# Optimization experiments

Measured on AMD Instinct MI355X. Metric: run time of the kernel, lower is better.

Reference implementation:

```python
import jax, jax.numpy as jnp
import numpy as np

B, N, K = 4, 65536, 16
HIDDEN = 64


def setup_inputs() -> dict:
    key = jax.random.key(0)
    k1, k2, k3, k4 = jax.random.split(key, 4)
    pos = jax.random.normal(k1, (B, 3, N), dtype=jnp.float32)
    idx = jax.random.randint(k2, (B, N, K), 0, N, dtype=jnp.int64)
    dist = jax.random.uniform(k3, (B, N, K), dtype=jnp.float32)
    W = jax.random.normal(k4, (10, HIDDEN), dtype=jnp.float32) * (1.0 / np.sqrt(10.0))
    b = jnp.zeros((HIDDEN,), dtype=jnp.float32)
    return {"pos": pos, "idx": idx, "dist": dist, "W": W, "b": b}


def reference(pos, idx, dist, W, b):
    xyz = pos[:, :3, :]                                  # [B, 3, N]
    # gather neighbor coords: neighbors[b, c, n, k] = xyz[b, c, idx[b, n, k]]
    neighbors = jax.vmap(lambda x, i: x[:, i])(xyz, idx)  # [B, 3, N, K]
    ext_xyz = jnp.broadcast_to(xyz[:, :, :, None], neighbors.shape)
    concat = jnp.concatenate(
        [ext_xyz, neighbors, ext_xyz - neighbors, dist[:, None, :, :]], axis=1
    )                                                    # [B, 10, N, K]
    feat = jnp.max(concat, axis=-1)                      # [B, 10, N]
    feat = jnp.transpose(feat, (0, 2, 1))                # [B, N, 10]
    return jax.nn.relu(feat @ W + b)                     # [B, N, HIDDEN]
```

## Files before the change

### kernel.cpp

```cpp
#include <hip/hip_runtime.h>

#define NPTS 65536
#define NB_SHIFT 16
#define HID 64

typedef float vfloat4 __attribute__((ext_vector_type(4)));
typedef int   vint4   __attribute__((ext_vector_type(4)));

__global__ __launch_bounds__(256) void xyzt_kernel(const float* __restrict__ pos,
                                                   vfloat4* __restrict__ xyzt) {
    int g = blockIdx.x * 256 + threadIdx.x;
    int b = g >> NB_SHIFT;
    int n = g & (NPTS - 1);
    const float* p = pos + (size_t)b * 3 * NPTS;
    vfloat4 v;
    v.x = p[n];
    v.y = p[n + NPTS];
    v.z = p[n + 2 * NPTS];
    v.w = 0.f;
    xyzt[((size_t)b << NB_SHIFT) + n] = v;
}

template <int USE_T>
__global__ __launch_bounds__(256, 4) void point_embed_kernel(
    const float*   __restrict__ pos,
    const vfloat4* __restrict__ xyzt,
    const int*     __restrict__ idx,
    const float*   __restrict__ dist,
    const float*   __restrict__ W,
    const float*   __restrict__ bias,
    float*         __restrict__ out) {
    __shared__ float featS[10][256];
    const int tid = threadIdx.x;

    const int blk = ((int)blockIdx.x & 7) * 128 + ((int)blockIdx.x >> 3);
    const int g = blk * 256 + tid;
    const int b = g >> NB_SHIFT;
    const int n = g & (NPTS - 1);

    const vint4* iv = (const vint4*)idx + (size_t)g * 4;
    vint4 i0 = iv[0], i1 = iv[1], i2 = iv[2], i3 = iv[3];

    float cx, cy, cz;
    float mxx = -INFINITY, mxy = -INFINITY, mxz = -INFINITY;
    float mnx = INFINITY, mny = INFINITY, mnz = INFINITY;
    float maxd;

    if (USE_T) {
        const vfloat4* xb = xyzt + ((size_t)b << NB_SHIFT);
        vfloat4 c = xb[n];
        vfloat4 q[16];
        q[0]  = xb[(unsigned)i0.x];
        q[1]  = xb[(unsigned)i0.y];
        q[2]  = xb[(unsigned)i0.z];
        q[3]  = xb[(unsigned)i0.w];
        q[4]  = xb[(unsigned)i1.x];
        q[5]  = xb[(unsigned)i1.y];
        q[6]  = xb[(unsigned)i1.z];
        q[7]  = xb[(unsigned)i1.w];
        q[8]  = xb[(unsigned)i2.x];
        q[9]  = xb[(unsigned)i2.y];
        q[10] = xb[(unsigned)i2.z];
        q[11] = xb[(unsigned)i2.w];
        q[12] = xb[(unsigned)i3.x];
        q[13] = xb[(unsigned)i3.y];
        q[14] = xb[(unsigned)i3.z];
        q[15] = xb[(unsigned)i3.w];

        const vfloat4* dv = (const vfloat4*)dist + (size_t)g * 4;
        vfloat4 d0 = dv[0], d1 = dv[1], d2 = dv[2], d3 = dv[3];
        maxd = fmaxf(
            fmaxf(fmaxf(fmaxf(d0.x, d0.y), fmaxf(d0.z, d0.w)),
                  fmaxf(fmaxf(d1.x, d1.y), fmaxf(d1.z, d1.w))),
            fmaxf(fmaxf(fmaxf(d2.x, d2.y), fmaxf(d2.z, d2.w)),
                  fmaxf(fmaxf(d3.x, d3.y), fmaxf(d3.z, d3.w))));

        cx = c.x; cy = c.y; cz = c.z;
#pragma unroll
        for (int j = 0; j < 16; ++j) {
            mxx = fmaxf(mxx, q[j].x);
            mxy = fmaxf(mxy, q[j].y);
            mxz = fmaxf(mxz, q[j].z);
            mnx = fminf(mnx, q[j].x);
            mny = fminf(mny, q[j].y);
            mnz = fminf(mnz, q[j].z);
        }
    } else {
        const float* px = pos + (size_t)b * 3 * NPTS;
        cx = px[n]; cy = px[n + NPTS]; cz = px[n + 2 * NPTS];
        const vfloat4* dv = (const vfloat4*)dist + (size_t)g * 4;
        vfloat4 d0 = dv[0], d1 = dv[1], d2 = dv[2], d3 = dv[3];
        maxd = fmaxf(
            fmaxf(fmaxf(fmaxf(d0.x, d0.y), fmaxf(d0.z, d0.w)),
                  fmaxf(fmaxf(d1.x, d1.y), fmaxf(d1.z, d1.w))),
            fmaxf(fmaxf(fmaxf(d2.x, d2.y), fmaxf(d2.z, d2.w)),
                  fmaxf(fmaxf(d3.x, d3.y), fmaxf(d3.z, d3.w))));
        int ids[16] = {i0.x, i0.y, i0.z, i0.w, i1.x, i1.y, i1.z, i1.w,
                       i2.x, i2.y, i2.z, i2.w, i3.x, i3.y, i3.z, i3.w};
#pragma unroll
        for (int j = 0; j < 16; ++j) {
            float qx = px[(unsigned)ids[j]];
            float qy = px[(unsigned)ids[j] + NPTS];
            float qz = px[(unsigned)ids[j] + 2 * NPTS];
            mxx = fmaxf(mxx, qx);
            mxy = fmaxf(mxy, qy);
            mxz = fmaxf(mxz, qz);
            mnx = fminf(mnx, qx);
            mny = fminf(mny, qy);
            mnz = fminf(mnz, qz);
        }
    }

    featS[0][tid] = cx;
    featS[1][tid] = cy;
    featS[2][tid] = cz;
    featS[3][tid] = mxx;
    featS[4][tid] = mxy;
    featS[5][tid] = mxz;
    featS[6][tid] = cx - mnx;
    featS[7][tid] = cy - mny;
    featS[8][tid] = cz - mnz;
    featS[9][tid] = maxd;

    const int hq = tid & 15;
    vfloat4 Wv[10];
#pragma unroll
    for (int c = 0; c < 10; ++c)
        Wv[c] = ((const vfloat4*)(W + c * HID))[hq];
    vfloat4 bv = ((const vfloat4*)bias)[hq];

    __syncthreads();

    const int prow = tid >> 4;
    const size_t outbase = (size_t)blk * 256 * HID;
#pragma unroll
    for (int i = 0; i < 16; ++i) {
        const int p = i * 16 + prow;
        vfloat4 acc = bv;
#pragma unroll
        for (int c = 0; c < 10; ++c) {
            const float fv = featS[c][p];
            acc.x += fv * Wv[c].x;
            acc.y += fv * Wv[c].y;
            acc.z += fv * Wv[c].z;
            acc.w += fv * Wv[c].w;
        }
        acc.x = fmaxf(acc.x, 0.f);
        acc.y = fmaxf(acc.y, 0.f);
        acc.z = fmaxf(acc.z, 0.f);
        acc.w = fmaxf(acc.w, 0.f);
        __builtin_nontemporal_store(
            acc, (vfloat4*)(out + outbase + (size_t)p * HID) + hq);
    }
}

extern "C" void kernel_launch(void* const* d_in, const int* in_sizes, int n_in,
                              void* d_out, int out_size, void* d_ws, size_t ws_size,
                              hipStream_t stream) {
    const float* pos  = (const float*)d_in[0];
    const int*   idx  = (const int*)d_in[1];
    const float* dist = (const float*)d_in[2];
    const float* W    = (const float*)d_in[3];
    const float* bias = (const float*)d_in[4];
    float* out = (float*)d_out;

    const int total   = in_sizes[0] / 3;
    const int nblocks = total / 256;
    const size_t need = (size_t)total * sizeof(vfloat4);

    if (ws_size >= need) {
        xyzt_kernel<<<nblocks, 256, 0, stream>>>(pos, (vfloat4*)d_ws);
        point_embed_kernel<1><<<nblocks, 256, 0, stream>>>(
            pos, (const vfloat4*)d_ws, idx, dist, W, bias, out);
    } else {
        point_embed_kernel<0><<<nblocks, 256, 0, stream>>>(
            pos, nullptr, idx, dist, W, bias, out);
    }
}
```

Measured before the change: 122.1 us.

## Split each point's 16 neighbors across 4 lanes with shuffle reductions

Each point is now handled by four threads instead of one. Each thread loads one int4 of indices and one float4 of distances and gathers four neighbors. Partial max and min values are combined with xor shuffles, and one lane writes the features to shared memory. Blocks now cover 64 points and the grid is four times larger. The aim is more memory-level parallelism and coalesced idx/dist loads. In exchange there is shuffle overhead, redundant center loads across the lanes, and a shorter output loop per block.

```diff
diff --git a/kernel.cpp b/kernel.cpp
--- a/kernel.cpp
+++ b/kernel.cpp
@@ -30,97 +30,76 @@
     const float*   __restrict__ W,
     const float*   __restrict__ bias,
     float*         __restrict__ out) {
-    __shared__ float featS[10][256];
+    __shared__ float featS[10][64];
     const int tid = threadIdx.x;
+    const int sub = tid & 3;
+    const int pl  = tid >> 2;
 
-    const int blk = ((int)blockIdx.x & 7) * 128 + ((int)blockIdx.x >> 3);
-    const int g = blk * 256 + tid;
+    const int blk = ((int)blockIdx.x & 7) * 512 + ((int)blockIdx.x >> 3);
+    const int g = blk * 64 + pl;
     const int b = g >> NB_SHIFT;
     const int n = g & (NPTS - 1);
 
-    const vint4* iv = (const vint4*)idx + (size_t)g * 4;
-    vint4 i0 = iv[0], i1 = iv[1], i2 = iv[2], i3 = iv[3];
+    vint4   iq = ((const vint4*)idx)[(size_t)g * 4 + sub];
+    vfloat4 dq = ((const vfloat4*)dist)[(size_t)g * 4 + sub];
 
     float cx, cy, cz;
-    float mxx = -INFINITY, mxy = -INFINITY, mxz = -INFINITY;
-    float mnx = INFINITY, mny = INFINITY, mnz = INFINITY;
-    float maxd;
+    float mxx, mxy, mxz, mnx, mny, mnz;
 
     if (USE_T) {
         const vfloat4* xb = xyzt + ((size_t)b << NB_SHIFT);
-        vfloat4 c = xb[n];
-        vfloat4 q[16];
-        q[0]  = xb[(unsigned)i0.x];
-        q[1]  = xb[(unsigned)i0.y];
-        q[2]  = xb[(unsigned)i0.z];
-        q[3]  = xb[(unsigned)i0.w];
-        q[4]  = xb[(unsigned)i1.x];
-        q[5]  = xb[(unsigned)i1.y];
-        q[6]  = xb[(unsigned)i1.z];
-        q[7]  = xb[(unsigned)i1.w];
-        q[8]  = xb[(unsigned)i2.x];
-        q[9]  = xb[(unsigned)i2.y];
-        q[10] = xb[(unsigned)i2.z];
-        q[11] = xb[(unsigned)i2.w];
-        q[12] = xb[(unsigned)i3.x];
-        q[13] = xb[(unsigned)i3.y];
-        q[14] = xb[(unsigned)i3.z];
-        q[15] = xb[(unsigned)i3.w];
-
-        const vfloat4* dv = (const vfloat4*)dist + (size_t)g * 4;
-        vfloat4 d0 = dv[0], d1 = dv[1], d2 = dv[2], d3 = dv[3];
-        maxd = fmaxf(
-            fmaxf(fmaxf(fmaxf(d0.x, d0.y), fmaxf(d0.z, d0.w)),
-                  fmaxf(fmaxf(d1.x, d1.y), fmaxf(d1.z, d1.w))),
-            fmaxf(fmaxf(fmaxf(d2.x, d2.y), fmaxf(d2.z, d2.w)),
-                  fmaxf(fmaxf(d3.x, d3.y), fmaxf(d3.z, d3.w))));
-
+        vfloat4 q0 = xb[(unsigned)iq.x];
+        vfloat4 q1 = xb[(unsigned)iq.y];
+        vfloat4 q2 = xb[(unsigned)iq.z];
+        vfloat4 q3 = xb[(unsigned)iq.w];
+        vfloat4 c  = xb[n];
         cx = c.x; cy = c.y; cz = c.z;
-#pragma unroll
-        for (int j = 0; j < 16; ++j) {
-            mxx = fmaxf(mxx, q[j].x);
-            mxy = fmaxf(mxy, q[j].y);
-            mxz = fmaxf(mxz, q[j].z);
-            mnx = fminf(mnx, q[j].x);
-            mny = fminf(mny, q[j].y);
-            mnz = fminf(mnz, q[j].z);
-        }
+        mxx = fmaxf(fmaxf(q0.x, q1.x), fmaxf(q2.x, q3.x));
+        mxy = fmaxf(fmaxf(q0.y, q1.y), fmaxf(q2.y, q3.y));
+        mxz = fmaxf(fmaxf(q0.z, q1.z), fmaxf(q2.z, q3.z));
+        mnx = fminf(fminf(q0.x, q1.x), fminf(q2.x, q3.x));
+        mny = fminf(fminf(q0.y, q1.y), fminf(q2.y, q3.y));
+        mnz = fminf(fminf(q0.z, q1.z), fminf(q2.z, q3.z));
     } else {
         const float* px = pos + (size_t)b * 3 * NPTS;
         cx = px[n]; cy = px[n + NPTS]; cz = px[n + 2 * NPTS];
-        const vfloat4* dv = (const vfloat4*)dist + (size_t)g * 4;
-        vfloat4 d0 = dv[0], d1 = dv[1], d2 = dv[2], d3 = dv[3];
-        maxd = fmaxf(
-            fmaxf(fmaxf(fmaxf(d0.x, d0.y), fmaxf(d0.z, d0.w)),
-                  fmaxf(fmaxf(d1.x, d1.y), fmaxf(d1.z, d1.w))),
-            fmaxf(fmaxf(fmaxf(d2.x, d2.y), fmaxf(d2.z, d2.w)),
-                  fmaxf(fmaxf(d3.x, d3.y), fmaxf(d3.z, d3.w))));
-        int ids[16] = {i0.x, i0.y, i0.z, i0.w, i1.x, i1.y, i1.z, i1.w,
-                       i2.x, i2.y, i2.z, i2.w, i3.x, i3.y, i3.z, i3.w};
+        mxx = mxy = mxz = -INFINITY;
+        mnx = mny = mnz = INFINITY;
+        int ids[4] = {iq.x, iq.y, iq.z, iq.w};
 #pragma unroll
-        for (int j = 0; j < 16; ++j) {
+        for (int j = 0; j < 4; ++j) {
             float qx = px[(unsigned)ids[j]];
             float qy = px[(unsigned)ids[j] + NPTS];
             float qz = px[(unsigned)ids[j] + 2 * NPTS];
-            mxx = fmaxf(mxx, qx);
-            mxy = fmaxf(mxy, qy);
-            mxz = fmaxf(mxz, qz);
-            mnx = fminf(mnx, qx);
-            mny = fminf(mny, qy);
-            mnz = fminf(mnz, qz);
+            mxx = fmaxf(mxx, qx); mxy = fmaxf(mxy, qy); mxz = fmaxf(mxz, qz);
+            mnx = fminf(mnx, qx); mny = fminf(mny, qy); mnz = fminf(mnz, qz);
         }
     }
+    float md = fmaxf(fmaxf(dq.x, dq.y), fmaxf(dq.z, dq.w));
 
-    featS[0][tid] = cx;
-    featS[1][tid] = cy;
-    featS[2][tid] = cz;
-    featS[3][tid] = mxx;
-    featS[4][tid] = mxy;
-    featS[5][tid] = mxz;
-    featS[6][tid] = cx - mnx;
-    featS[7][tid] = cy - mny;
-    featS[8][tid] = cz - mnz;
-    featS[9][tid] = maxd;
+#pragma unroll
+    for (int m = 1; m <= 2; m <<= 1) {
+        mxx = fmaxf(mxx, __shfl_xor(mxx, m));
+        mxy = fmaxf(mxy, __shfl_xor(mxy, m));
+        mxz = fmaxf(mxz, __shfl_xor(mxz, m));
+        mnx = fminf(mnx, __shfl_xor(mnx, m));
+        mny = fminf(mny, __shfl_xor(mny, m));
+        mnz = fminf(mnz, __shfl_xor(mnz, m));
+        md  = fmaxf(md,  __shfl_xor(md,  m));
+    }
+
+    if (sub == 0) {
+        featS[0][pl] = cx;
+        featS[1][pl] = cy;
+        featS[2][pl] = cz;
+        featS[3][pl] = mxx;
+        featS[4][pl] = mxy;
+        featS[5][pl] = mxz;
+        featS[6][pl] = cx - mnx;
+        featS[7][pl] = cy - mny;
+        featS[8][pl] = cz - mnz;
+        featS[9][pl] = md;
+    }
 
     const int hq = tid & 15;
     vfloat4 Wv[10];
@@ -132,9 +111,9 @@
     __syncthreads();
 
     const int prow = tid >> 4;
-    const size_t outbase = (size_t)blk * 256 * HID;
+    const size_t outbase = (size_t)blk * 64 * HID;
 #pragma unroll
-    for (int i = 0; i < 16; ++i) {
+    for (int i = 0; i < 4; ++i) {
         const int p = i * 16 + prow;
         vfloat4 acc = bv;
 #pragma unroll
@@ -164,16 +143,15 @@
     const float* bias = (const float*)d_in[4];
     float* out = (float*)d_out;
 
-    const int total   = in_sizes[0] / 3;
-    const int nblocks = total / 256;
+    const int total = in_sizes[0] / 3;
     const size_t need = (size_t)total * sizeof(vfloat4);
 
     if (ws_size >= need) {
-        xyzt_kernel<<<nblocks, 256, 0, stream>>>(pos, (vfloat4*)d_ws);
-        point_embed_kernel<1><<<nblocks, 256, 0, stream>>>(
+        xyzt_kernel<<<total / 256, 256, 0, stream>>>(pos, (vfloat4*)d_ws);
+        point_embed_kernel<1><<<total / 64, 256, 0, stream>>>(
             pos, (const vfloat4*)d_ws, idx, dist, W, bias, out);
     } else {
-        point_embed_kernel<0><<<nblocks, 256, 0, stream>>>(
+        point_embed_kernel<0><<<total / 64, 256, 0, stream>>>(
             pos, nullptr, idx, dist, W, bias, out);
     }
 }
```

Result: slower. 128.8 us (+5.4%).
